# Performance work log

Measured on AMD Instinct MI355X. Metric: run time of the kernel, lower is better.

## Reference

```python
import jax, jax.numpy as jnp
import numpy as np


def setup_inputs() -> dict:
    key = jax.random.key(0)
    B, m, n = 2048, 256, 64
    y = jax.random.normal(key, (B, 2 * m, n), dtype=jnp.float32)
    return {"y": y}


def reference(y):
    # y: [B, 2m, n], real part stacked over imaginary part along axis 1.
    B, two_m, n = y.shape
    m = two_m // 2
    yR = y[:, :m, :]   # [B, m, n]
    yI = y[:, m:, :]   # [B, m, n]

    def outer(carry, i):
        QR, QI = carry                      # [B, m, n] each
        yRi = jnp.take(yR, i, axis=2)       # [B, m] original column i
        yIi = jnp.take(yI, i, axis=2)

        def inner(qc, j):
            qR, qI = qc
            QRj = jnp.take(QR, j, axis=2)   # [B, m]
            QIj = jnp.take(QI, j, axis=2)
            # rij = <qR, QRj> + <qI, QIj>  (as in the original code)
            rij = (jnp.sum(qR * QRj, axis=1, keepdims=True)
                   + jnp.sum(qI * QIj, axis=1, keepdims=True))  # [B, 1]
            # Faithful quirk: subtract projection from the ORIGINAL column.
            nqR = yRi - rij * QRj
            nqI = yIi - rij * QIj
            valid = j < i
            qR = jnp.where(valid, nqR, qR)
            qI = jnp.where(valid, nqI, qI)
            return (qR, qI), None

        (qR, qI), _ = jax.lax.scan(inner, (yRi, yIi), jnp.arange(n))
        # Faithful quirk: normalize by SQUARED norm of the original column.
        denom = jnp.sum(yRi * yRi + yIi * yIi, axis=1, keepdims=True)  # [B, 1]
        QR = QR.at[:, :, i].set(qR / denom)
        QI = QI.at[:, :, i].set(qI / denom)
        return (QR, QI), None

    init = (jnp.zeros_like(yR), jnp.zeros_like(yI))
    (QR, QI), _ = jax.lax.scan(outer, init, jnp.arange(n))
    return jnp.concatenate([QR, QI], axis=1)  # [B, 2m, n]
```

## Files before the change

kernel.cpp:

```cpp
#include <hip/hip_runtime.h>

#define TWO_M 512
#define NCOL  64
#define SK    136
#define SKW   68
#define SG    68

typedef short short8 __attribute__((ext_vector_type(8)));
typedef float f32x4  __attribute__((ext_vector_type(4)));

static __device__ __forceinline__ unsigned int f2bf(float f) {
    unsigned int u = __builtin_bit_cast(unsigned int, f);
    return (u + 0x7fffu + ((u >> 16) & 1u)) >> 16;
}
static __device__ __forceinline__ float bflo(unsigned int p) {
    return __builtin_bit_cast(float, p << 16);
}
static __device__ __forceinline__ float bfhi(unsigned int p) {
    return __builtin_bit_cast(float, p & 0xffff0000u);
}

#define FRAGP(base, row, k0) (*(const short8*)&(base)[(row) * SK + ((((k0) >> 3) ^ (((row) >> 2) & 7)) << 3)])

__global__ __launch_bounds__(512, 4) void gs_fused(const float* __restrict__ y,
                                                   float* __restrict__ out)
{
    __shared__ __align__(16) unsigned char smem[35840];
    unsigned short* Yt0 = (unsigned short*)smem;
    unsigned short* Yt1 = (unsigned short*)(smem + 17408);
    unsigned int*   Yw0 = (unsigned int*)smem;
    unsigned int*   Yw1 = (unsigned int*)(smem + 17408);
    float*          Gl  = (float*)smem;
    float*          bd  = (float*)(smem + 34816);

    const int   batch = blockIdx.x;
    const float* Y    = y + (size_t)batch * (TWO_M * NCOL);
    const int   tid   = threadIdx.x;
    const int   wave  = tid >> 6;
    const int   lane  = tid & 63;
    const int   cq    = tid & 15;

    f32x4 acc0 = {0, 0, 0, 0}, acc1 = {0, 0, 0, 0};
    const int arow = 16 * (wave >> 1) + (lane & 15);
    const int bc0  = 32 * (wave & 1) + (lane & 15);
    const int koff = (lane >> 4) * 8;

    const int kp0 = tid >> 4;
    const int kp1 = 32 + kp0;
    const int ws0 = ((((kp0 >> 2) ^ (cq & 7)) << 2) | (kp0 & 3));
    const int ws1 = ((((kp1 >> 2) ^ (cq & 7)) << 2) | (kp1 & 3));
    const int c0r = 4 * cq;
    const int ia0 = kp0 * 32 + cq, ib0 = kp0 * 32 + 16 + cq;
    const int ia1 = kp1 * 32 + cq, ib1 = kp1 * 32 + 16 + cq;

    unsigned int pk[4][8];

    float4 va0, vb0, va1, vb1;
    {
        const float4* src = (const float4*)Y;
        va0 = src[ia0]; vb0 = src[ib0];
        va1 = src[ia1]; vb1 = src[ib1];
    }
#pragma unroll
    for (int c = 0; c < 4; ++c) {
        pk[c][0] = f2bf(va0.x) | (f2bf(vb0.x) << 16);
        pk[c][1] = f2bf(va0.y) | (f2bf(vb0.y) << 16);
        pk[c][2] = f2bf(va0.z) | (f2bf(vb0.z) << 16);
        pk[c][3] = f2bf(va0.w) | (f2bf(vb0.w) << 16);
        pk[c][4] = f2bf(va1.x) | (f2bf(vb1.x) << 16);
        pk[c][5] = f2bf(va1.y) | (f2bf(vb1.y) << 16);
        pk[c][6] = f2bf(va1.z) | (f2bf(vb1.z) << 16);
        pk[c][7] = f2bf(va1.w) | (f2bf(vb1.w) << 16);
        if (c < 3) {
            const float4* src = (const float4*)(Y + (size_t)(c + 1) * 128 * NCOL);
            va0 = src[ia0]; vb0 = src[ib0];
            va1 = src[ia1]; vb1 = src[ib1];
        }
        unsigned int* Yw = (c & 1) ? Yw1 : Yw0;
#pragma unroll
        for (int j = 0; j < 4; ++j) {
            Yw[(c0r + j) * SKW + ws0] = pk[c][j];
            Yw[(c0r + j) * SKW + ws1] = pk[c][4 + j];
        }
        __syncthreads();
        const unsigned short* Yt = (c & 1) ? Yt1 : Yt0;
#pragma unroll
        for (int kb = 0; kb < 128; kb += 32) {
            const short8 af  = FRAGP(Yt, arow, kb + koff);
            const short8 bf0 = FRAGP(Yt, bc0, kb + koff);
            const short8 bf1 = FRAGP(Yt, bc0 + 16, kb + koff);
            acc0 = __builtin_amdgcn_mfma_f32_16x16x32_bf16(af, bf0, acc0, 0, 0, 0);
            acc1 = __builtin_amdgcn_mfma_f32_16x16x32_bf16(af, bf1, acc1, 0, 0, 0);
        }
    }

#pragma unroll
    for (int j = 0; j < 4; ++j) {
        const int gr = 16 * (wave >> 1) + (lane >> 4) * 4 + j;
        Gl[gr * SG + 32 * (wave & 1) + (lane & 15)]      = acc0[j];
        Gl[gr * SG + 32 * (wave & 1) + 16 + (lane & 15)] = acc1[j];
    }
    __syncthreads();

    if (wave == 0) {
        const int l = lane;
        const float d     = Gl[l * SG + l];
        const float invd  = 1.0f / d;
        const float invd0 = __shfl(invd, 0);
        float T  = Gl[l] * invd0;
        float r  = T;
        float Nq = __shfl(T, 0) * invd0;
        float bj = __shfl(r, 1);
        float bsave = 0.f;
        float grow = Gl[SG + l];
        for (int j = 1; j < 64; ++j) {
            const float grow_next = Gl[(j < 63 ? j + 1 : 63) * SG + l];
            const float invdj = __shfl(invd, j);
            const float Tprev = T;
            T = (grow - bj * Tprev) * invdj;
            const float cj = (__shfl(Tprev, j) - bj * Nq) * invdj;
            Nq = (__shfl(T, j) - bj * cj) * invdj;
            r  = T - r * cj;
            if (l == j) bsave = bj;
            bj = __shfl(r, (j + 1) & 63);
            grow = grow_next;
        }
        bd[l]      = -bsave * invd;
        bd[64 + l] = invd;
    }
    __syncthreads();

    const float a0 = bd[c0r],      a1 = bd[c0r + 1];
    const float a2 = bd[c0r + 2],  a3 = bd[c0r + 3];
    const float i0 = bd[64 + c0r],     i1 = bd[64 + c0r + 1];
    const float i2 = bd[64 + c0r + 2], i3 = bd[64 + c0r + 3];
    f32x4* o4 = (f32x4*)(out + (size_t)batch * (TWO_M * NCOL));

#pragma unroll
    for (int c = 0; c < 4; ++c) {
#pragma unroll
        for (int pr = 0; pr < 2; ++pr) {
            const int rbase = 128 * c + 2 * (pr ? kp1 : kp0);
            const unsigned int u0 = pk[c][4 * pr + 0];
            const unsigned int u1 = pk[c][4 * pr + 1];
            const unsigned int u2 = pk[c][4 * pr + 2];
            const unsigned int u3 = pk[c][4 * pr + 3];
#pragma unroll
            for (int h = 0; h < 2; ++h) {
                const float y0 = h ? bfhi(u0) : bflo(u0);
                const float y1 = h ? bfhi(u1) : bflo(u1);
                const float y2 = h ? bfhi(u2) : bflo(u2);
                const float y3 = h ? bfhi(u3) : bflo(u3);
                const float b0 = y0 * i0, b1 = y1 * i1, b2 = y2 * i2, b3 = y3 * i3;
                float A = a0, C = b0;
                A = a1 * A; C = fmaf(a1, C, b1);
                A = a2 * A; C = fmaf(a2, C, b2);
                A = a3 * A; C = fmaf(a3, C, b3);
#pragma unroll
                for (int dlt = 1; dlt < 16; dlt <<= 1) {
                    const float Ap = __shfl_up(A, dlt, 16);
                    const float Cp = __shfl_up(C, dlt, 16);
                    const bool ok = (cq >= dlt);
                    C = ok ? fmaf(A, Cp, C) : C;
                    A = ok ? (A * Ap) : A;
                }
                float qin = __shfl_up(C, 1, 16);
                if (cq == 0) qin = 0.f;
                const float q0 = fmaf(a0, qin, b0);
                const float q1 = fmaf(a1, q0, b1);
                const float q2 = fmaf(a2, q1, b2);
                const float q3 = fmaf(a3, q2, b3);
                __builtin_nontemporal_store(f32x4{q0, q1, q2, q3},
                                            &o4[(rbase + h) * 16 + cq]);
            }
        }
    }
}

extern "C" void kernel_launch(void* const* d_in, const int* in_sizes, int n_in,
                              void* d_out, int out_size, void* d_ws, size_t ws_size,
                              hipStream_t stream)
{
    const float* y = (const float*)d_in[0];
    float* out = (float*)d_out;
    const int B = in_sizes[0] / (TWO_M * NCOL);
    gs_fused<<<dim3(B), dim3(512), 0, stream>>>(y, out);
}
```

Before: 94.26 us.

## Replicate serial recurrence in every wave and prefetch two chunks ahead

Every wave now runs the 64-step Gram recurrence redundantly and gets its coefficients through lane shuffles. This removes the shared-memory broadcast buffer and the block barrier that left seven waves idle while wave 0 computed. The load pipeline is also unrolled by hand so that global loads run two chunks ahead, using two register sets instead of one. The cost is redundant ALU and LDS reads in all waves and higher register pressure.

Result: slower. 101.0 us (+7.2%).

```diff
diff --git a/kernel.cpp b/kernel.cpp
--- a/kernel.cpp
+++ b/kernel.cpp
@@ -25,13 +25,12 @@
 __global__ __launch_bounds__(512, 4) void gs_fused(const float* __restrict__ y,
                                                    float* __restrict__ out)
 {
-    __shared__ __align__(16) unsigned char smem[35840];
+    __shared__ __align__(16) unsigned char smem[34816];
     unsigned short* Yt0 = (unsigned short*)smem;
     unsigned short* Yt1 = (unsigned short*)(smem + 17408);
     unsigned int*   Yw0 = (unsigned int*)smem;
     unsigned int*   Yw1 = (unsigned int*)(smem + 17408);
     float*          Gl  = (float*)smem;
-    float*          bd  = (float*)(smem + 34816);
 
     const int   batch = blockIdx.x;
     const float* Y    = y + (size_t)batch * (TWO_M * NCOL);
@@ -55,44 +54,56 @@
 
     unsigned int pk[4][8];
 
-    float4 va0, vb0, va1, vb1;
-    {
-        const float4* src = (const float4*)Y;
-        va0 = src[ia0]; vb0 = src[ib0];
-        va1 = src[ia1]; vb1 = src[ib1];
+    const float4* s4 = (const float4*)Y;
+
+    float4 A0 = s4[ia0], A1 = s4[ib0], A2 = s4[ia1], A3 = s4[ib1];
+    float4 B0 = s4[2048 + ia0], B1 = s4[2048 + ib0], B2 = s4[2048 + ia1], B3 = s4[2048 + ib1];
+
+#define PK(c, R0, R1, R2, R3)                                          \
+    pk[c][0] = f2bf(R0.x) | (f2bf(R1.x) << 16);                        \
+    pk[c][1] = f2bf(R0.y) | (f2bf(R1.y) << 16);                        \
+    pk[c][2] = f2bf(R0.z) | (f2bf(R1.z) << 16);                        \
+    pk[c][3] = f2bf(R0.w) | (f2bf(R1.w) << 16);                        \
+    pk[c][4] = f2bf(R2.x) | (f2bf(R3.x) << 16);                        \
+    pk[c][5] = f2bf(R2.y) | (f2bf(R3.y) << 16);                        \
+    pk[c][6] = f2bf(R2.z) | (f2bf(R3.z) << 16);                        \
+    pk[c][7] = f2bf(R2.w) | (f2bf(R3.w) << 16);
+
+#define DSW(c, Yw)                                                     \
+    _Pragma("unroll")                                                  \
+    for (int j = 0; j < 4; ++j) {                                      \
+        (Yw)[(c0r + j) * SKW + ws0] = pk[c][j];                        \
+        (Yw)[(c0r + j) * SKW + ws1] = pk[c][4 + j];                    \
     }
-#pragma unroll
-    for (int c = 0; c < 4; ++c) {
-        pk[c][0] = f2bf(va0.x) | (f2bf(vb0.x) << 16);
-        pk[c][1] = f2bf(va0.y) | (f2bf(vb0.y) << 16);
-        pk[c][2] = f2bf(va0.z) | (f2bf(vb0.z) << 16);
-        pk[c][3] = f2bf(va0.w) | (f2bf(vb0.w) << 16);
-        pk[c][4] = f2bf(va1.x) | (f2bf(vb1.x) << 16);
-        pk[c][5] = f2bf(va1.y) | (f2bf(vb1.y) << 16);
-        pk[c][6] = f2bf(va1.z) | (f2bf(vb1.z) << 16);
-        pk[c][7] = f2bf(va1.w) | (f2bf(vb1.w) << 16);
-        if (c < 3) {
-            const float4* src = (const float4*)(Y + (size_t)(c + 1) * 128 * NCOL);
-            va0 = src[ia0]; vb0 = src[ib0];
-            va1 = src[ia1]; vb1 = src[ib1];
-        }
-        unsigned int* Yw = (c & 1) ? Yw1 : Yw0;
-#pragma unroll
-        for (int j = 0; j < 4; ++j) {
-            Yw[(c0r + j) * SKW + ws0] = pk[c][j];
-            Yw[(c0r + j) * SKW + ws1] = pk[c][4 + j];
-        }
-        __syncthreads();
-        const unsigned short* Yt = (c & 1) ? Yt1 : Yt0;
-#pragma unroll
-        for (int kb = 0; kb < 128; kb += 32) {
-            const short8 af  = FRAGP(Yt, arow, kb + koff);
-            const short8 bf0 = FRAGP(Yt, bc0, kb + koff);
-            const short8 bf1 = FRAGP(Yt, bc0 + 16, kb + koff);
-            acc0 = __builtin_amdgcn_mfma_f32_16x16x32_bf16(af, bf0, acc0, 0, 0, 0);
-            acc1 = __builtin_amdgcn_mfma_f32_16x16x32_bf16(af, bf1, acc1, 0, 0, 0);
-        }
+
+#define MFMA_STEP(Yt)                                                  \
+    _Pragma("unroll")                                                  \
+    for (int kb = 0; kb < 128; kb += 32) {                             \
+        const short8 af  = FRAGP(Yt, arow, kb + koff);                 \
+        const short8 bf0 = FRAGP(Yt, bc0, kb + koff);                  \
+        const short8 bf1 = FRAGP(Yt, bc0 + 16, kb + koff);             \
+        acc0 = __builtin_amdgcn_mfma_f32_16x16x32_bf16(af, bf0, acc0, 0, 0, 0); \
+        acc1 = __builtin_amdgcn_mfma_f32_16x16x32_bf16(af, bf1, acc1, 0, 0, 0); \
     }
+
+    PK(0, A0, A1, A2, A3);
+    A0 = s4[4096 + ia0]; A1 = s4[4096 + ib0]; A2 = s4[4096 + ia1]; A3 = s4[4096 + ib1];
+    DSW(0, Yw0);
+    __syncthreads();
+    MFMA_STEP(Yt0);
+    PK(1, B0, B1, B2, B3);
+    B0 = s4[6144 + ia0]; B1 = s4[6144 + ib0]; B2 = s4[6144 + ia1]; B3 = s4[6144 + ib1];
+    DSW(1, Yw1);
+    __syncthreads();
+    MFMA_STEP(Yt1);
+    PK(2, A0, A1, A2, A3);
+    DSW(2, Yw0);
+    __syncthreads();
+    MFMA_STEP(Yt0);
+    PK(3, B0, B1, B2, B3);
+    DSW(3, Yw1);
+    __syncthreads();
+    MFMA_STEP(Yt1);
 
 #pragma unroll
     for (int j = 0; j < 4; ++j) {
@@ -102,10 +113,11 @@
     }
     __syncthreads();
 
-    if (wave == 0) {
+    float alpha, invd;
+    {
         const int l = lane;
         const float d     = Gl[l * SG + l];
-        const float invd  = 1.0f / d;
+        invd = 1.0f / d;
         const float invd0 = __shfl(invd, 0);
         float T  = Gl[l] * invd0;
         float r  = T;
@@ -125,15 +137,14 @@
             bj = __shfl(r, (j + 1) & 63);
             grow = grow_next;
         }
-        bd[l]      = -bsave * invd;
-        bd[64 + l] = invd;
+        alpha = -bsave * invd;
     }
-    __syncthreads();
 
-    const float a0 = bd[c0r],      a1 = bd[c0r + 1];
-    const float a2 = bd[c0r + 2],  a3 = bd[c0r + 3];
-    const float i0 = bd[64 + c0r],     i1 = bd[64 + c0r + 1];
-    const float i2 = bd[64 + c0r + 2], i3 = bd[64 + c0r + 3];
+    const float a0 = __shfl(alpha, c0r),     a1 = __shfl(alpha, c0r + 1);
+    const float a2 = __shfl(alpha, c0r + 2), a3 = __shfl(alpha, c0r + 3);
+    const float i0 = __shfl(invd, c0r),      i1 = __shfl(invd, c0r + 1);
+    const float i2 = __shfl(invd, c0r + 2),  i3 = __shfl(invd, c0r + 3);
+
     f32x4* o4 = (f32x4*)(out + (size_t)batch * (TWO_M * NCOL));
 
 #pragma unroll
```

## Process two batches per block with software-pipelined Gram and output phases

Applied to the files above, without the earlier changes.

Each block now handles two batch elements. The second batch's global loads, bf16 packing and Gram-matrix MFMAs run interleaved with the first batch's prefix-scan output stores. This is meant to overlap the serial recurrence and store phase with compute and loads, and to halve the block count. It doubles the packed register state per thread, which may raise register pressure or cause spills under the existing launch bounds, and it assumes an even batch count.

Result: slower. 120.0 us (+27.3%).

```diff
diff --git a/kernel.cpp b/kernel.cpp
--- a/kernel.cpp
+++ b/kernel.cpp
@@ -5,6 +5,7 @@
 #define SK    136
 #define SKW   68
 #define SG    68
+#define BSTRIDE (TWO_M * NCOL)
 
 typedef short short8 __attribute__((ext_vector_type(8)));
 typedef float f32x4  __attribute__((ext_vector_type(4)));
@@ -22,8 +23,97 @@
 
 #define FRAGP(base, row, k0) (*(const short8*)&(base)[(row) * SK + ((((k0) >> 3) ^ (((row) >> 2) & 7)) << 3)])
 
-__global__ __launch_bounds__(512, 4) void gs_fused(const float* __restrict__ y,
-                                                   float* __restrict__ out)
+#define PK(PKA, c, R0, R1, R2, R3)                                     \
+    PKA[c][0] = f2bf(R0.x) | (f2bf(R1.x) << 16);                       \
+    PKA[c][1] = f2bf(R0.y) | (f2bf(R1.y) << 16);                       \
+    PKA[c][2] = f2bf(R0.z) | (f2bf(R1.z) << 16);                       \
+    PKA[c][3] = f2bf(R0.w) | (f2bf(R1.w) << 16);                       \
+    PKA[c][4] = f2bf(R2.x) | (f2bf(R3.x) << 16);                       \
+    PKA[c][5] = f2bf(R2.y) | (f2bf(R3.y) << 16);                       \
+    PKA[c][6] = f2bf(R2.z) | (f2bf(R3.z) << 16);                       \
+    PKA[c][7] = f2bf(R2.w) | (f2bf(R3.w) << 16);
+
+#define DSW(PKA, c, Yw)                                                \
+    _Pragma("unroll")                                                  \
+    for (int j = 0; j < 4; ++j) {                                      \
+        (Yw)[(c0r + j) * SKW + ws0] = PKA[c][j];                       \
+        (Yw)[(c0r + j) * SKW + ws1] = PKA[c][4 + j];                   \
+    }
+
+#define MFMA_STEP(Yt)                                                  \
+    _Pragma("unroll")                                                  \
+    for (int kb = 0; kb < 128; kb += 32) {                             \
+        const short8 af  = FRAGP(Yt, arow, kb + koff);                 \
+        const short8 bf0 = FRAGP(Yt, bc0, kb + koff);                  \
+        const short8 bf1 = FRAGP(Yt, bc0 + 16, kb + koff);             \
+        acc0 = __builtin_amdgcn_mfma_f32_16x16x32_bf16(af, bf0, acc0, 0, 0, 0); \
+        acc1 = __builtin_amdgcn_mfma_f32_16x16x32_bf16(af, bf1, acc1, 0, 0, 0); \
+    }
+
+#define P3UNIT(PKA, c, pr, h, A0_, A1_, A2_, A3_, I0_, I1_, I2_, I3_, O4_) \
+    {                                                                  \
+        const int rbase = 128 * (c) + 2 * ((pr) ? kp1 : kp0);          \
+        const unsigned int u0 = PKA[c][4 * (pr) + 0];                  \
+        const unsigned int u1 = PKA[c][4 * (pr) + 1];                  \
+        const unsigned int u2 = PKA[c][4 * (pr) + 2];                  \
+        const unsigned int u3 = PKA[c][4 * (pr) + 3];                  \
+        const float y0 = (h) ? bfhi(u0) : bflo(u0);                    \
+        const float y1 = (h) ? bfhi(u1) : bflo(u1);                    \
+        const float y2 = (h) ? bfhi(u2) : bflo(u2);                    \
+        const float y3 = (h) ? bfhi(u3) : bflo(u3);                    \
+        const float b0 = y0 * I0_, b1 = y1 * I1_, b2 = y2 * I2_, b3 = y3 * I3_; \
+        float A = A0_, C = b0;                                         \
+        A = A1_ * A; C = fmaf(A1_, C, b1);                             \
+        A = A2_ * A; C = fmaf(A2_, C, b2);                             \
+        A = A3_ * A; C = fmaf(A3_, C, b3);                             \
+        _Pragma("unroll")                                              \
+        for (int dlt = 1; dlt < 16; dlt <<= 1) {                       \
+            const float Ap = __shfl_up(A, dlt, 16);                    \
+            const float Cp = __shfl_up(C, dlt, 16);                    \
+            const bool ok = (cq >= dlt);                               \
+            C = ok ? fmaf(A, Cp, C) : C;                               \
+            A = ok ? (A * Ap) : A;                                     \
+        }                                                              \
+        float qin = __shfl_up(C, 1, 16);                               \
+        if (cq == 0) qin = 0.f;                                        \
+        const float q0 = fmaf(A0_, qin, b0);                           \
+        const float q1 = fmaf(A1_, q0, b1);                            \
+        const float q2 = fmaf(A2_, q1, b2);                            \
+        const float q3 = fmaf(A3_, q2, b3);                            \
+        __builtin_nontemporal_store(f32x4{q0, q1, q2, q3},             \
+                                    &(O4_)[(rbase + (h)) * 16 + cq]);  \
+    }
+
+#define RECURRENCE(bds)                                                \
+    if (wave == 0) {                                                   \
+        const int l = lane;                                            \
+        const float d     = Gl[l * SG + l];                            \
+        const float invd  = 1.0f / d;                                  \
+        const float invd0 = __shfl(invd, 0);                           \
+        float T  = Gl[l] * invd0;                                      \
+        float r  = T;                                                  \
+        float Nq = __shfl(T, 0) * invd0;                               \
+        float bj = __shfl(r, 1);                                       \
+        float bsave = 0.f;                                             \
+        float grow = Gl[SG + l];                                       \
+        for (int j = 1; j < 64; ++j) {                                 \
+            const float grow_next = Gl[(j < 63 ? j + 1 : 63) * SG + l];\
+            const float invdj = __shfl(invd, j);                       \
+            const float Tprev = T;                                     \
+            T = (grow - bj * Tprev) * invdj;                           \
+            const float cj = (__shfl(Tprev, j) - bj * Nq) * invdj;     \
+            Nq = (__shfl(T, j) - bj * cj) * invdj;                     \
+            r  = T - r * cj;                                           \
+            if (l == j) bsave = bj;                                    \
+            bj = __shfl(r, (j + 1) & 63);                              \
+            grow = grow_next;                                          \
+        }                                                              \
+        (bds)[l]      = -bsave * invd;                                 \
+        (bds)[64 + l] = invd;                                          \
+    }
+
+__global__ __launch_bounds__(512, 4) void gs_fused2(const float* __restrict__ y,
+                                                    float* __restrict__ out)
 {
     __shared__ __align__(16) unsigned char smem[35840];
     unsigned short* Yt0 = (unsigned short*)smem;
@@ -31,16 +121,14 @@
     unsigned int*   Yw0 = (unsigned int*)smem;
     unsigned int*   Yw1 = (unsigned int*)(smem + 17408);
     float*          Gl  = (float*)smem;
-    float*          bd  = (float*)(smem + 34816);
-
-    const int   batch = blockIdx.x;
-    const float* Y    = y + (size_t)batch * (TWO_M * NCOL);
-    const int   tid   = threadIdx.x;
-    const int   wave  = tid >> 6;
-    const int   lane  = tid & 63;
-    const int   cq    = tid & 15;
-
-    f32x4 acc0 = {0, 0, 0, 0}, acc1 = {0, 0, 0, 0};
+    float*          bd0 = (float*)(smem + 34816);
+    float*          bd1 = (float*)(smem + 35328);
+
+    const int tid  = threadIdx.x;
+    const int wave = tid >> 6;
+    const int lane = tid & 63;
+    const int cq   = tid & 15;
+
     const int arow = 16 * (wave >> 1) + (lane & 15);
     const int bc0  = 32 * (wave & 1) + (lane & 15);
     const int koff = (lane >> 4) * 8;
@@ -53,47 +141,35 @@
     const int ia0 = kp0 * 32 + cq, ib0 = kp0 * 32 + 16 + cq;
     const int ia1 = kp1 * 32 + cq, ib1 = kp1 * 32 + 16 + cq;
 
-    unsigned int pk[4][8];
-
-    float4 va0, vb0, va1, vb1;
-    {
-        const float4* src = (const float4*)Y;
-        va0 = src[ia0]; vb0 = src[ib0];
-        va1 = src[ia1]; vb1 = src[ib1];
-    }
+    const float* Y0 = y + (size_t)(2 * blockIdx.x) * BSTRIDE;
+    const float* Y1 = Y0 + BSTRIDE;
+    f32x4* o40 = (f32x4*)(out + (size_t)(2 * blockIdx.x) * BSTRIDE);
+    f32x4* o41 = o40 + (BSTRIDE / 4);
+
+    unsigned int pk0[4][8], pk1[4][8];
+    f32x4 acc0 = {0, 0, 0, 0}, acc1 = {0, 0, 0, 0};
+
+    const float4* s4 = (const float4*)Y0;
+    float4 va0 = s4[ia0], vb0 = s4[ib0], va1 = s4[ia1], vb1 = s4[ib1];
 #pragma unroll
     for (int c = 0; c < 4; ++c) {
-        pk[c][0] = f2bf(va0.x) | (f2bf(vb0.x) << 16);
-        pk[c][1] = f2bf(va0.y) | (f2bf(vb0.y) << 16);
-        pk[c][2] = f2bf(va0.z) | (f2bf(vb0.z) << 16);
-        pk[c][3] = f2bf(va0.w) | (f2bf(vb0.w) << 16);
-        pk[c][4] = f2bf(va1.x) | (f2bf(vb1.x) << 16);
-        pk[c][5] = f2bf(va1.y) | (f2bf(vb1.y) << 16);
-        pk[c][6] = f2bf(va1.z) | (f2bf(vb1.z) << 16);
-        pk[c][7] = f2bf(va1.w) | (f2bf(vb1.w) << 16);
+        PK(pk0, c, va0, vb0, va1, vb1);
         if (c < 3) {
-            const float4* src = (const float4*)(Y + (size_t)(c + 1) * 128 * NCOL);
+            const float4* src = (const float4*)(Y0 + (size_t)(c + 1) * 128 * NCOL);
+            va0 = src[ia0]; vb0 = src[ib0];
+            va1 = src[ia1]; vb1 = src[ib1];
+        }
+        if (c == 3) {
+            const float4* src = (const float4*)Y1;
             va0 = src[ia0]; vb0 = src[ib0];
             va1 = src[ia1]; vb1 = src[ib1];
         }
         unsigned int* Yw = (c & 1) ? Yw1 : Yw0;
-#pragma unroll
-        for (int j = 0; j < 4; ++j) {
-            Yw[(c0r + j) * SKW + ws0] = pk[c][j];
-            Yw[(c0r + j) * SKW + ws1] = pk[c][4 + j];
-        }
+        DSW(pk0, c, Yw);
         __syncthreads();
         const unsigned short* Yt = (c & 1) ? Yt1 : Yt0;
-#pragma unroll
-        for (int kb = 0; kb < 128; kb += 32) {
-            const short8 af  = FRAGP(Yt, arow, kb + koff);
-            const short8 bf0 = FRAGP(Yt, bc0, kb + koff);
-            const short8 bf1 = FRAGP(Yt, bc0 + 16, kb + koff);
-            acc0 = __builtin_amdgcn_mfma_f32_16x16x32_bf16(af, bf0, acc0, 0, 0, 0);
-            acc1 = __builtin_amdgcn_mfma_f32_16x16x32_bf16(af, bf1, acc1, 0, 0, 0);
-        }
-    }
-
+        MFMA_STEP(Yt);
+    }
 #pragma unroll
     for (int j = 0; j < 4; ++j) {
         const int gr = 16 * (wave >> 1) + (lane >> 4) * 4 + j;
@@ -101,79 +177,54 @@
         Gl[gr * SG + 32 * (wave & 1) + 16 + (lane & 15)] = acc1[j];
     }
     __syncthreads();
-
-    if (wave == 0) {
-        const int l = lane;
-        const float d     = Gl[l * SG + l];
-        const float invd  = 1.0f / d;
-        const float invd0 = __shfl(invd, 0);
-        float T  = Gl[l] * invd0;
-        float r  = T;
-        float Nq = __shfl(T, 0) * invd0;
-        float bj = __shfl(r, 1);
-        float bsave = 0.f;
-        float grow = Gl[SG + l];
-        for (int j = 1; j < 64; ++j) {
-            const float grow_next = Gl[(j < 63 ? j + 1 : 63) * SG + l];
-            const float invdj = __shfl(invd, j);
-            const float Tprev = T;
-            T = (grow - bj * Tprev) * invdj;
-            const float cj = (__shfl(Tprev, j) - bj * Nq) * invdj;
-            Nq = (__shfl(T, j) - bj * cj) * invdj;
-            r  = T - r * cj;
-            if (l == j) bsave = bj;
-            bj = __shfl(r, (j + 1) & 63);
-            grow = grow_next;
+    RECURRENCE(bd0);
+    __syncthreads();
+
+    const float a00 = bd0[c0r],      a01 = bd0[c0r + 1];
+    const float a02 = bd0[c0r + 2],  a03 = bd0[c0r + 3];
+    const float i00 = bd0[64 + c0r],     i01 = bd0[64 + c0r + 1];
+    const float i02 = bd0[64 + c0r + 2], i03 = bd0[64 + c0r + 3];
+
+    acc0 = f32x4{0, 0, 0, 0}; acc1 = f32x4{0, 0, 0, 0};
+#pragma unroll
+    for (int c = 0; c < 4; ++c) {
+        PK(pk1, c, va0, vb0, va1, vb1);
+        if (c < 3) {
+            const float4* src = (const float4*)(Y1 + (size_t)(c + 1) * 128 * NCOL);
+            va0 = src[ia0]; vb0 = src[ib0];
+            va1 = src[ia1]; vb1 = src[ib1];
         }
-        bd[l]      = -bsave * invd;
-        bd[64 + l] = invd;
-    }
-    __syncthreads();
-
-    const float a0 = bd[c0r],      a1 = bd[c0r + 1];
-    const float a2 = bd[c0r + 2],  a3 = bd[c0r + 3];
-    const float i0 = bd[64 + c0r],     i1 = bd[64 + c0r + 1];
-    const float i2 = bd[64 + c0r + 2], i3 = bd[64 + c0r + 3];
-    f32x4* o4 = (f32x4*)(out + (size_t)batch * (TWO_M * NCOL));
+        unsigned int* Yw = (c & 1) ? Yw1 : Yw0;
+        DSW(pk1, c, Yw);
+        __syncthreads();
+        const unsigned short* Yt = (c & 1) ? Yt1 : Yt0;
+        MFMA_STEP(Yt);
+        P3UNIT(pk0, c, 0, 0, a00, a01, a02, a03, i00, i01, i02, i03, o40);
+        P3UNIT(pk0, c, 0, 1, a00, a01, a02, a03, i00, i01, i02, i03, o40);
+        P3UNIT(pk0, c, 1, 0, a00, a01, a02, a03, i00, i01, i02, i03, o40);
+        P3UNIT(pk0, c, 1, 1, a00, a01, a02, a03, i00, i01, i02, i03, o40);
+    }
+#pragma unroll
+    for (int j = 0; j < 4; ++j) {
+        const int gr = 16 * (wave >> 1) + (lane >> 4) * 4 + j;
+        Gl[gr * SG + 32 * (wave & 1) + (lane & 15)]      = acc0[j];
+        Gl[gr * SG + 32 * (wave & 1) + 16 + (lane & 15)] = acc1[j];
+    }
+    __syncthreads();
+    RECURRENCE(bd1);
+    __syncthreads();
+
+    const float a10 = bd1[c0r],      a11 = bd1[c0r + 1];
+    const float a12 = bd1[c0r + 2],  a13 = bd1[c0r + 3];
+    const float i10 = bd1[64 + c0r],     i11 = bd1[64 + c0r + 1];
+    const float i12 = bd1[64 + c0r + 2], i13 = bd1[64 + c0r + 3];
 
 #pragma unroll
     for (int c = 0; c < 4; ++c) {
-#pragma unroll
-        for (int pr = 0; pr < 2; ++pr) {
-            const int rbase = 128 * c + 2 * (pr ? kp1 : kp0);
-            const unsigned int u0 = pk[c][4 * pr + 0];
-            const unsigned int u1 = pk[c][4 * pr + 1];
-            const unsigned int u2 = pk[c][4 * pr + 2];
-            const unsigned int u3 = pk[c][4 * pr + 3];
-#pragma unroll
-            for (int h = 0; h < 2; ++h) {
-                const float y0 = h ? bfhi(u0) : bflo(u0);
-                const float y1 = h ? bfhi(u1) : bflo(u1);
-                const float y2 = h ? bfhi(u2) : bflo(u2);
-                const float y3 = h ? bfhi(u3) : bflo(u3);
-                const float b0 = y0 * i0, b1 = y1 * i1, b2 = y2 * i2, b3 = y3 * i3;
-                float A = a0, C = b0;
-                A = a1 * A; C = fmaf(a1, C, b1);
-                A = a2 * A; C = fmaf(a2, C, b2);
-                A = a3 * A; C = fmaf(a3, C, b3);
-#pragma unroll
-                for (int dlt = 1; dlt < 16; dlt <<= 1) {
-                    const float Ap = __shfl_up(A, dlt, 16);
-                    const float Cp = __shfl_up(C, dlt, 16);
-                    const bool ok = (cq >= dlt);
-                    C = ok ? fmaf(A, Cp, C) : C;
-                    A = ok ? (A * Ap) : A;
-                }
-                float qin = __shfl_up(C, 1, 16);
-                if (cq == 0) qin = 0.f;
-                const float q0 = fmaf(a0, qin, b0);
-                const float q1 = fmaf(a1, q0, b1);
-                const float q2 = fmaf(a2, q1, b2);
-                const float q3 = fmaf(a3, q2, b3);
-                __builtin_nontemporal_store(f32x4{q0, q1, q2, q3},
-                                            &o4[(rbase + h) * 16 + cq]);
-            }
-        }
+        P3UNIT(pk1, c, 0, 0, a10, a11, a12, a13, i10, i11, i12, i13, o41);
+        P3UNIT(pk1, c, 0, 1, a10, a11, a12, a13, i10, i11, i12, i13, o41);
+        P3UNIT(pk1, c, 1, 0, a10, a11, a12, a13, i10, i11, i12, i13, o41);
+        P3UNIT(pk1, c, 1, 1, a10, a11, a12, a13, i10, i11, i12, i13, o41);
     }
 }
 
@@ -183,6 +234,6 @@
 {
     const float* y = (const float*)d_in[0];
     float* out = (float*)d_out;
-    const int B = in_sizes[0] / (TWO_M * NCOL);
-    gs_fused<<<dim3(B), dim3(512), 0, stream>>>(y, out);
-}
+    const int B = in_sizes[0] / BSTRIDE;
+    gs_fused2<<<dim3(B / 2), dim3(512), 0, stream>>>(y, out);
+}
```
